# Kernel optimization log

Hardware: AMD Instinct MI355X
Metric: run time of the kernel (lower is better)

## Reference

```python
import jax, jax.numpy as jnp
import numpy as np

B, L, D, K = 16, 512, 512, 8
D2 = 2 * D
KS = 9
PAD = (KS - 1) // 2
EPS = 1e-5


def _conv_block(x, w, b, g, beta):
    # x: [B, L, D]; conv over time dim with 'same' padding, then LayerNorm over D, ReLU
    y = jax.lax.conv_general_dilated(
        x.transpose(0, 2, 1), w, window_strides=(1,), padding=[(PAD, PAD)],
        dimension_numbers=('NCH', 'OIH', 'NCH'))
    y = y.transpose(0, 2, 1) + b  # [B, L, D]
    mean = jnp.mean(y, axis=-1, keepdims=True)
    var = jnp.var(y, axis=-1, keepdims=True)
    y = (y - mean) * jax.lax.rsqrt(var + EPS) * g + beta
    return jax.nn.relu(y)


def _gru_scan(x, w_ih, w_hh, b_ih, b_hh):
    # x: [B, L, D]; torch GRUCell math, input = concat(x_t, h_{t-1}) per module
    def step(h, x_t):
        p = jnp.concatenate([x_t, h], axis=-1)          # [B, D + D2]
        gi = p @ w_ih.T + b_ih                          # [B, 3*D2]
        gh = h @ w_hh.T + b_hh
        ir, iz, inn = jnp.split(gi, 3, axis=-1)
        hr, hz, hn = jnp.split(gh, 3, axis=-1)
        r = jax.nn.sigmoid(ir + hr)
        z = jax.nn.sigmoid(iz + hz)
        n = jnp.tanh(inn + r * hn)
        h_new = (1.0 - z) * n + z * h
        return h_new, h_new

    h0 = jnp.zeros((x.shape[0], w_hh.shape[1]), x.dtype)
    _, hs = jax.lax.scan(step, h0, x.transpose(1, 0, 2))  # [L, B, D2]
    return hs.transpose(1, 0, 2)                           # [B, L, D2]


def setup_inputs() -> dict:
    key = jax.random.key(0)
    ks = jax.random.split(key, 12)
    n = lambda k, sh, s=0.02: jax.random.normal(k, sh, dtype=jnp.float32) * s
    return {
        'h_text': jax.random.normal(ks[0], (B, L, D), dtype=jnp.float32),
        'conv1_w': n(ks[1], (D, D, KS)), 'conv1_b': jnp.zeros((D,), jnp.float32),
        'ln1_g': jnp.ones((D,), jnp.float32), 'ln1_b': jnp.zeros((D,), jnp.float32),
        'conv2_w': n(ks[2], (D, D, KS)), 'conv2_b': jnp.zeros((D,), jnp.float32),
        'ln2_g': jnp.ones((D,), jnp.float32), 'ln2_b': jnp.zeros((D,), jnp.float32),
        'w_ih': n(ks[3], (3 * D2, D + D2)), 'w_hh': n(ks[4], (3 * D2, D2)),
        'b_ih': jnp.zeros((3 * D2,), jnp.float32), 'b_hh': jnp.zeros((3 * D2,), jnp.float32),
        'mdn_w_w': n(ks[5], (K, D2)), 'mdn_w_b': jnp.zeros((K,), jnp.float32),
        'mdn_sigma_w': n(ks[6], (K * D2, D2)), 'mdn_sigma_b': jnp.zeros((K * D2,), jnp.float32),
        'mdn_mu_w': n(ks[7], (K * D2, D2)), 'mdn_mu_b': jnp.zeros((K * D2,), jnp.float32),
    }


def reference(h_text, conv1_w, conv1_b, ln1_g, ln1_b, conv2_w, conv2_b, ln2_g, ln2_b,
              w_ih, w_hh, b_ih, b_hh, mdn_w_w, mdn_w_b, mdn_sigma_w, mdn_sigma_b,
              mdn_mu_w, mdn_mu_b):
    x = _conv_block(h_text, conv1_w, conv1_b, ln1_g, ln1_b)
    x = _conv_block(x, conv2_w, conv2_b, ln2_g, ln2_b)
    h = _gru_scan(x, w_ih, w_hh, b_ih, b_hh)                 # [B, L, 2D]
    w = jax.nn.softmax(h @ mdn_w_w.T + mdn_w_b, axis=-1)     # [B, L, K]
    sigma = jnp.exp(h @ mdn_sigma_w.T + mdn_sigma_b).reshape(B, L, K, D2)
    mu = (h @ mdn_mu_w.T + mdn_mu_b).reshape(B, L, K, D2)
    return (w, sigma, mu)
```

## Files before the change

kernel.cpp:

```cpp
#include <hip/hip_runtime.h>
#include <hip/hip_bf16.h>
#include <math.h>

#define BB 16
#define LL 512
#define DD 512
#define DD2 1024
#define KMIX 8
#define LPAD 520
#define GRU_KSTEPS 33

typedef __attribute__((ext_vector_type(8))) short short8;
typedef __attribute__((ext_vector_type(4))) float f32x4;
typedef unsigned short ushort;

__device__ __forceinline__ float bf2f(ushort u) {
  union { float f; unsigned i; } v; v.i = ((unsigned)u) << 16; return v.f;
}
__device__ __forceinline__ ushort f2bf(float f) {
  union { float f; unsigned i; } v; v.f = f;
  unsigned i = v.i;
  unsigned r = i + 0x7FFF + ((i >> 16) & 1);
  return (ushort)(r >> 16);
}

__global__ void k_zero_bf16(ushort* p, long n) {
  for (long i = blockIdx.x * 256 + threadIdx.x; i < n; i += (long)gridDim.x * 256) p[i] = 0;
}
__global__ void k_fill_xpad(const float* __restrict__ x, ushort* __restrict__ xp) {
  const long n = (long)BB * LPAD * DD;
  for (long i = blockIdx.x * 256 + threadIdx.x; i < n; i += (long)gridDim.x * 256) {
    int d = (int)(i & 511);
    long rest = i >> 9;
    int p = (int)(rest % LPAD);
    int b = (int)(rest / LPAD);
    float v = 0.f;
    if (p >= 4 && p < 516) v = x[((long)b * LL + (p - 4)) * DD + d];
    xp[i] = f2bf(v);
  }
}
__global__ void k_pack_convw(const float* __restrict__ w, ushort* __restrict__ wp) {
  const long n = (long)DD * DD * 9;
  for (long idx = blockIdx.x * 256 + threadIdx.x; idx < n; idx += (long)gridDim.x * 256) {
    int i = (int)(idx & 511);
    int o = (int)((idx >> 9) & 511);
    int k = (int)(idx >> 18);
    wp[idx] = f2bf(w[((long)o * DD + i) * 9 + k]);
  }
}
__global__ void k_pack_wihx(const float* __restrict__ w_ih, ushort* __restrict__ wp) {
  const long n = (long)3 * DD2 * DD;
  for (long idx = blockIdx.x * 256 + threadIdx.x; idx < n; idx += (long)gridDim.x * 256) {
    int i = (int)(idx & 511);
    int nr = (int)(idx >> 9);
    wp[idx] = f2bf(w_ih[(long)nr * 1536 + i]);
  }
}
__global__ void k_pack_bf16(const float* __restrict__ s, ushort* __restrict__ d, long n) {
  for (long i = blockIdx.x * 256 + threadIdx.x; i < n; i += (long)gridDim.x * 256) d[i] = f2bf(s[i]);
}
__global__ void k_pack_gru(const float* __restrict__ w_ih, const float* __restrict__ w_hh,
                           const float* __restrict__ b_hh, ushort* __restrict__ wp) {
  const long n = (long)64 * 6 * GRU_KSTEPS * 64 * 8;
  for (long idx = blockIdx.x * 256 + threadIdx.x; idx < n; idx += (long)gridDim.x * 256) {
    int j = (int)(idx & 7);
    int lane = (int)((idx >> 3) & 63);
    long r9 = idx >> 9;
    int ks = (int)(r9 % GRU_KSTEPS);
    long tmp = r9 / GRU_KSTEPS;
    int s = (int)(tmp % 6);
    int blk = (int)(tmp / 6);
    int k = ks * 32 + ((lane >> 4) << 3) + j;
    int u = blk * 16 + (lane & 15);
    float v = 0.f;
    if (s < 3) {
      if (k < 1024) v = w_ih[((long)(s * DD2 + u)) * 1536 + 512 + k];
    } else {
      int nr = (s - 3) * DD2 + u;
      if (k < 1024) v = w_hh[(long)nr * DD2 + k];
      else if (k == 1024) v = b_hh[nr];
    }
    wp[idx] = f2bf(v);
  }
}
__global__ void k_init_hbuf(ushort* hb, unsigned* flags) {
  int i = blockIdx.x * 256 + threadIdx.x;
  if (i < 16384) hb[i] = 0;
  if (i < 1024) flags[i] = 0u;
}

template <int MODE, int AMAP>
__global__ __launch_bounds__(256) void gemm128(
    const ushort* __restrict__ A, int lda, long segAoff,
    const ushort* __restrict__ Bt, int ldb, long segBoff,
    int nseg, int kseg, void* __restrict__ Cout, int ldc,
    const float* __restrict__ bias) {
  __shared__ ushort As[128 * 64];
  __shared__ ushort Bs[128 * 64];
  const int tid = threadIdx.x, lane = tid & 63, w = tid >> 6;
  const int wr = w >> 1, wc = w & 1;
  const int m0 = blockIdx.y * 128, n0 = blockIdx.x * 128;

  const ushort* Abase;
  if (AMAP == 1) {
    int b = m0 >> 9, l = m0 & 511;
    Abase = A + ((long)(b * LPAD + l)) * DD;
  } else {
    Abase = A + (long)m0 * lda;
  }
  const ushort* Bbase = Bt + (long)n0 * ldb;

  f32x4 acc[4][4];
#pragma unroll
  for (int i = 0; i < 4; i++)
#pragma unroll
    for (int j = 0; j < 4; j++) acc[i][j] = {0.f, 0.f, 0.f, 0.f};

  for (int seg = 0; seg < nseg; ++seg) {
    const ushort* Aseg = Abase + (long)seg * segAoff;
    const ushort* Bseg = Bbase + (long)seg * segBoff;
    for (int k0 = 0; k0 < kseg; k0 += 64) {
#pragma unroll
      for (int it = 0; it < 4; ++it) {
        int chunk = it * 256 + tid;
        int r = chunk >> 3, cc = chunk & 7;
        int sc = cc ^ (r & 7);
        *(short8*)&As[(size_t)chunk * 8] = *(const short8*)(Aseg + (long)r * lda + k0 + sc * 8);
        *(short8*)&Bs[(size_t)chunk * 8] = *(const short8*)(Bseg + (long)r * ldb + k0 + sc * 8);
      }
      __syncthreads();
#pragma unroll
      for (int kk = 0; kk < 2; ++kk) {
        short8 af[4], bfv[4];
#pragma unroll
        for (int m = 0; m < 4; m++) {
          int row = wr * 64 + m * 16 + (lane & 15);
          int ch = (kk * 4 + (lane >> 4)) ^ (row & 7);
          af[m] = *(const short8*)&As[(size_t)(row * 8 + ch) * 8];
        }
#pragma unroll
        for (int nn = 0; nn < 4; nn++) {
          int row = wc * 64 + nn * 16 + (lane & 15);
          int ch = (kk * 4 + (lane >> 4)) ^ (row & 7);
          bfv[nn] = *(const short8*)&Bs[(size_t)(row * 8 + ch) * 8];
        }
#pragma unroll
        for (int m = 0; m < 4; m++)
#pragma unroll
          for (int nn = 0; nn < 4; nn++)
            acc[m][nn] = __builtin_amdgcn_mfma_f32_16x16x32_bf16(af[m], bfv[nn], acc[m][nn], 0, 0, 0);
      }
      __syncthreads();
    }
  }
  float bvals[4];
#pragma unroll
  for (int nn = 0; nn < 4; nn++) {
    int c = n0 + wc * 64 + nn * 16 + (lane & 15);
    bvals[nn] = bias[c];
  }
#pragma unroll
  for (int m = 0; m < 4; m++) {
    int rbase = m0 + wr * 64 + m * 16 + ((lane >> 4) << 2);
#pragma unroll
    for (int nn = 0; nn < 4; nn++) {
      int c = n0 + wc * 64 + nn * 16 + (lane & 15);
#pragma unroll
      for (int j = 0; j < 4; j++) {
        float v = acc[m][nn][j] + bvals[nn];
        long off = (long)(rbase + j) * ldc + c;
        if (MODE == 0) ((float*)Cout)[off] = v;
        else {
          int r = rbase + j;
          int bb = r >> 9, tt = r & 511, ss = c >> 10, uu = c & 1023;
          long o2 = ((((long)(tt * 64 + (uu >> 4))) * 3 + ss) << 8) + (bb << 4) + (uu & 15);
          ((ushort*)Cout)[o2] = f2bf(v);
        }
      }
    }
  }
}

template <int DSTPAD>
__global__ __launch_bounds__(256) void ln_relu(
    const float* __restrict__ y, const float* __restrict__ g,
    const float* __restrict__ be, ushort* __restrict__ dst) {
  const int r = blockIdx.x, tid = threadIdx.x;
  float v0 = y[(long)r * DD + tid];
  float v1 = y[(long)r * DD + 256 + tid];
  float s = v0 + v1, sq = v0 * v0 + v1 * v1;
#pragma unroll
  for (int o = 32; o; o >>= 1) { s += __shfl_down(s, o); sq += __shfl_down(sq, o); }
  __shared__ float red[8];
  int w = tid >> 6, lane = tid & 63;
  if (lane == 0) { red[w] = s; red[4 + w] = sq; }
  __syncthreads();
  if (tid == 0) {
    float ts = 0.f, tq = 0.f;
#pragma unroll
    for (int i = 0; i < 4; i++) { ts += red[i]; tq += red[4 + i]; }
    red[0] = ts; red[1] = tq;
  }
  __syncthreads();
  float mean = red[0] * (1.f / 512.f);
  float var = red[1] * (1.f / 512.f) - mean * mean;
  float rs = rsqrtf(var + 1e-5f);
  long dbase;
  if (DSTPAD) { int b = r >> 9, l = r & 511; dbase = ((long)(b * LPAD + l + 4)) * DD; }
  else dbase = (long)r * DD;
  float o0 = fmaxf(0.f, (v0 - mean) * rs * g[tid] + be[tid]);
  float o1 = fmaxf(0.f, (v1 - mean) * rs * g[tid + 256] + be[tid + 256]);
  dst[dbase + tid] = f2bf(o0);
  dst[dbase + 256 + tid] = f2bf(o1);
}

__device__ __forceinline__ void wait_flags(unsigned need, int tid,
                                           const unsigned* __restrict__ flags) {
  if ((tid >> 6) == 0) {
    while (1) {
      unsigned f = __hip_atomic_load(&flags[(tid & 63) << 4], __ATOMIC_RELAXED,
                                     __HIP_MEMORY_SCOPE_AGENT);
      if (__all((int)(f >= need))) break;
      __builtin_amdgcn_s_sleep(127);
    }
  }
  __syncthreads();
}

__device__ void do_pair(int m0, int n0,
                        const ushort* __restrict__ A,
                        const ushort* __restrict__ Bsg, const ushort* __restrict__ Bmu,
                        const float* __restrict__ sg_b, const float* __restrict__ mu_b,
                        float* __restrict__ Cs, float* __restrict__ Cm,
                        char* smem, int tid) {
  ushort* As = (ushort*)smem;
  ushort* B1 = As + 128 * 64;
  ushort* B2 = B1 + 128 * 64;
  const int lane = tid & 63, w = tid >> 6;
  const int wr = w >> 2, wc = w & 3;
  const ushort* Abase = A + (long)m0 * DD2;
  const ushort* Bsb = Bsg + (long)n0 * DD2;
  const ushort* Bmb = Bmu + (long)n0 * DD2;
  f32x4 accS[4][2], accM[4][2];
#pragma unroll
  for (int m = 0; m < 4; m++)
#pragma unroll
    for (int n = 0; n < 2; n++) { accS[m][n] = {0.f,0.f,0.f,0.f}; accM[m][n] = {0.f,0.f,0.f,0.f}; }

  for (int k0 = 0; k0 < DD2; k0 += 64) {
#pragma unroll
    for (int it = 0; it < 2; ++it) {
      int chunk = it * 512 + tid;
      int r = chunk >> 3, cc = chunk & 7, sc = cc ^ (r & 7);
      *(short8*)&As[(size_t)chunk * 8] = *(const short8*)(Abase + (long)r * DD2 + k0 + sc * 8);
      *(short8*)&B1[(size_t)chunk * 8] = *(const short8*)(Bsb + (long)r * DD2 + k0 + sc * 8);
      *(short8*)&B2[(size_t)chunk * 8] = *(const short8*)(Bmb + (long)r * DD2 + k0 + sc * 8);
    }
    __syncthreads();
#pragma unroll
    for (int kk = 0; kk < 2; ++kk) {
      short8 af[4], b1[2], b2[2];
#pragma unroll
      for (int m = 0; m < 4; m++) {
        int row = wr * 64 + m * 16 + (lane & 15);
        int ch = (kk * 4 + (lane >> 4)) ^ (row & 7);
        af[m] = *(const short8*)&As[(size_t)(row * 8 + ch) * 8];
      }
#pragma unroll
      for (int n = 0; n < 2; n++) {
        int row = wc * 32 + n * 16 + (lane & 15);
        int ch = (kk * 4 + (lane >> 4)) ^ (row & 7);
        b1[n] = *(const short8*)&B1[(size_t)(row * 8 + ch) * 8];
        b2[n] = *(const short8*)&B2[(size_t)(row * 8 + ch) * 8];
      }
#pragma unroll
      for (int m = 0; m < 4; m++)
#pragma unroll
        for (int n = 0; n < 2; n++) {
          accS[m][n] = __builtin_amdgcn_mfma_f32_16x16x32_bf16(af[m], b1[n], accS[m][n], 0, 0, 0);
          accM[m][n] = __builtin_amdgcn_mfma_f32_16x16x32_bf16(af[m], b2[n], accM[m][n], 0, 0, 0);
        }
    }
    __syncthreads();
  }
  const int ldc = KMIX * DD2;
#pragma unroll
  for (int n = 0; n < 2; n++) {
    const int c = n0 + wc * 32 + n * 16 + (lane & 15);
    const float bs = sg_b[c], bm = mu_b[c];
#pragma unroll
    for (int m = 0; m < 4; m++) {
      const int rbase = m0 + wr * 64 + m * 16 + ((lane >> 4) << 2);
#pragma unroll
      for (int j = 0; j < 4; j++) {
        const long off = (long)(rbase + j) * ldc + c;
        Cs[off] = expf(accS[m][n][j] + bs);
        Cm[off] = accM[m][n][j] + bm;
      }
    }
  }
}

__global__ __launch_bounds__(512, 2) void fused_scan_mdn(
    const ushort* __restrict__ Wp, const ushort* __restrict__ gix2,
    const float* __restrict__ b_hh,
    ushort* __restrict__ hbuf, ushort* __restrict__ h_seq,
    unsigned* __restrict__ flags,
    const ushort* __restrict__ mdnsg, const ushort* __restrict__ mdnmu,
    const float* __restrict__ sg_b, const float* __restrict__ mu_b,
    float* __restrict__ outS, float* __restrict__ outM) {
  __shared__ char smem[49152];
  const int tid = threadIdx.x;

  if (blockIdx.x < 64) {
    float* red = (float*)smem;
    const int lane = tid & 63, w = tid >> 6, blk = blockIdx.x;
    const int j_c = w;
    const int u_local = lane & 15;
    const int b = ((lane >> 4) << 2) + (j_c & 3);
    const int u = (blk << 4) + u_local;
    const int lanep = ((blk & 1) * 2 + (u_local >> 3)) * 16 + b;
    const long hout_off = ((long)(blk >> 1) * 64 + lanep) * 8 + (u_local & 7);
    const ushort* wpw = Wp + (long)blk * 6 * GRU_KSTEPS * 512 + (long)lane * 8;
    const float bhr = b_hh[u], bhz = b_hh[DD2 + u], bhn = b_hh[2 * DD2 + u];
    float hold = 0.f;

    short8 wr0[4], wr1[4], wr2[4], wr3[4], wr4[4], wr5[4];
#pragma unroll
    for (int i = 0; i < 4; ++i) {
      const int ks = i * 8 + w;
      wr0[i] = *(const short8*)(wpw + (long)(0 * GRU_KSTEPS + ks) * 512);
      wr1[i] = *(const short8*)(wpw + (long)(1 * GRU_KSTEPS + ks) * 512);
      wr2[i] = *(const short8*)(wpw + (long)(2 * GRU_KSTEPS + ks) * 512);
      wr3[i] = *(const short8*)(wpw + (long)(3 * GRU_KSTEPS + ks) * 512);
      wr4[i] = *(const short8*)(wpw + (long)(4 * GRU_KSTEPS + ks) * 512);
      wr5[i] = *(const short8*)(wpw + (long)(5 * GRU_KSTEPS + ks) * 512);
    }

    const int gofs = (b << 4) + u_local;
    for (int t = 0; t < LL; ++t) {
      float gx_r = 0.f, gx_z = 0.f, gx_n = 0.f;
      if (w < 4) {
        const long gbase = ((long)(t * 64 + blk) * 3) << 8;
        gx_r = bf2f(__builtin_nontemporal_load(gix2 + gbase + gofs));
        gx_z = bf2f(__builtin_nontemporal_load(gix2 + gbase + 256 + gofs));
        gx_n = bf2f(__builtin_nontemporal_load(gix2 + gbase + 512 + gofs));
      }
      if (t > 0) {
        if (w == 0) {
          const unsigned tgt = (unsigned)t;
          while (1) {
            unsigned f = __hip_atomic_load(&flags[lane << 4], __ATOMIC_RELAXED,
                                           __HIP_MEMORY_SCOPE_AGENT);
            if (__all((int)(f >= tgt))) break;
            __builtin_amdgcn_s_sleep(1);
          }
        }
        __syncthreads();
      }

      const ushort* hb = hbuf + ((long)t << 14);
      f32x4 acc0 = {0.f,0.f,0.f,0.f}, acc1 = acc0, acc2 = acc0,
            acc3 = acc0, acc4 = acc0, acc5 = acc0;
#pragma unroll
      for (int i = 0; i < 4; ++i) {
        const int ks = i * 8 + w;
        unsigned long long* ap = (unsigned long long*)(hb + (((long)ks * 64 + lane) << 3));
        union { unsigned long long q[2]; short8 v; } cv;
        cv.q[0] = __hip_atomic_load(ap,     __ATOMIC_RELAXED, __HIP_MEMORY_SCOPE_AGENT);
        cv.q[1] = __hip_atomic_load(ap + 1, __ATOMIC_RELAXED, __HIP_MEMORY_SCOPE_AGENT);
        acc0 = __builtin_amdgcn_mfma_f32_16x16x32_bf16(cv.v, wr0[i], acc0, 0, 0, 0);
        acc1 = __builtin_amdgcn_mfma_f32_16x16x32_bf16(cv.v, wr1[i], acc1, 0, 0, 0);
        acc2 = __builtin_amdgcn_mfma_f32_16x16x32_bf16(cv.v, wr2[i], acc2, 0, 0, 0);
        acc3 = __builtin_amdgcn_mfma_f32_16x16x32_bf16(cv.v, wr3[i], acc3, 0, 0, 0);
        acc4 = __builtin_amdgcn_mfma_f32_16x16x32_bf16(cv.v, wr4[i], acc4, 0, 0, 0);
        acc5 = __builtin_amdgcn_mfma_f32_16x16x32_bf16(cv.v, wr5[i], acc5, 0, 0, 0);
      }
#pragma unroll
      for (int j = 0; j < 4; ++j) {
        red[((w * 6 + 0) << 8) + (j << 6) + lane] = acc0[j];
        red[((w * 6 + 1) << 8) + (j << 6) + lane] = acc1[j];
        red[((w * 6 + 2) << 8) + (j << 6) + lane] = acc2[j];
        red[((w * 6 + 3) << 8) + (j << 6) + lane] = acc3[j];
        red[((w * 6 + 4) << 8) + (j << 6) + lane] = acc4[j];
        red[((w * 6 + 5) << 8) + (j << 6) + lane] = acc5[j];
      }
      __syncthreads();
      ushort h16 = 0;
      if (w < 4) {
        float v0 = 0.f, v1 = 0.f, v2 = 0.f, v3 = 0.f, v4 = 0.f, v5 = 0.f;
#pragma unroll
        for (int wv = 0; wv < 8; ++wv) {
          const int base = ((wv * 6) << 8) + (j_c << 6) + lane;
          v0 += red[base];
          v1 += red[base + 256];
          v2 += red[base + 512];
          v3 += red[base + 768];
          v4 += red[base + 1024];
          v5 += red[base + 1280];
        }
        const float rg = 1.f / (1.f + __expf(-(gx_r + v0 + v3 + bhr)));
        const float zg = 1.f / (1.f + __expf(-(gx_z + v1 + v4 + bhz)));
        const float nx = gx_n + v2 + rg * (v5 + bhn);
        const float ng = 1.f - 2.f / (__expf(2.f * nx) + 1.f);
        const float hn = (1.f - zg) * ng + zg * hold;
        hold = hn;
        h16 = f2bf(hn);
      }
      if (t < LL - 1) {
        if (w < 4)
          __hip_atomic_store(hbuf + (((long)(t + 1)) << 14) + hout_off, h16,
                             __ATOMIC_RELAXED, __HIP_MEMORY_SCOPE_AGENT);
        __syncthreads();
        if (tid == 0)
          __hip_atomic_store(&flags[blk << 4], (unsigned)(t + 1), __ATOMIC_RELAXED,
                             __HIP_MEMORY_SCOPE_AGENT);
      }
      if (w < 4)
        __hip_atomic_store(h_seq + ((long)b * LL + t) * DD2 + u, h16,
                           __ATOMIC_RELAXED, __HIP_MEMORY_SCOPE_AGENT);
    }
    __syncthreads();
    if (tid == 0)
      __hip_atomic_store(&flags[blk << 4], 600u, __ATOMIC_RELAXED,
                         __HIP_MEMORY_SCOPE_AGENT);
  } else {
    const int wid = blockIdx.x - 64;
    for (int i = wid; i < 3072; i += 192) {
      const int nb = i & 63;
      const int rest = i >> 6;
      const int b = rest & 15;
      const int t0 = (rest >> 4) * 128;
      wait_flags((unsigned)(t0 + 129), tid, flags);
      do_pair(b * 512 + t0, nb * 128, h_seq, mdnsg, mdnmu, sg_b, mu_b,
              outS, outM, smem, tid);
    }
  }
  for (int i = blockIdx.x; i < 1024; i += 256) {
    const int nb = i & 63;
    const int b = (i >> 6) & 15;
    wait_flags(513u, tid, flags);
    do_pair(b * 512 + 384, nb * 128, h_seq, mdnsg, mdnmu, sg_b, mu_b,
            outS, outM, smem, tid);
  }
}

__global__ __launch_bounds__(256) void w_head(
    const ushort* __restrict__ h_seq, const float* __restrict__ ww,
    const float* __restrict__ wb, float* __restrict__ out) {
  const int tid = threadIdx.x, lane = tid & 63, w = tid >> 6;
  const long r = (long)blockIdx.x * 4 + w;
  float s[KMIX];
#pragma unroll
  for (int k = 0; k < KMIX; k++) s[k] = 0.f;
  for (int u = lane; u < DD2; u += 64) {
    float hv = bf2f(h_seq[r * DD2 + u]);
#pragma unroll
    for (int k = 0; k < KMIX; k++) s[k] += hv * ww[(long)k * DD2 + u];
  }
#pragma unroll
  for (int k = 0; k < KMIX; k++)
#pragma unroll
    for (int o = 32; o; o >>= 1) s[k] += __shfl_xor(s[k], o);
#pragma unroll
  for (int k = 0; k < KMIX; k++) s[k] += wb[k];
  float m = s[0];
#pragma unroll
  for (int k = 1; k < KMIX; k++) m = fmaxf(m, s[k]);
  float esum = 0.f;
#pragma unroll
  for (int k = 0; k < KMIX; k++) { s[k] = expf(s[k] - m); esum += s[k]; }
  float mine = 0.f;
#pragma unroll
  for (int k = 0; k < KMIX; k++) if (lane == k) mine = s[k];
  if (lane < KMIX) out[r * KMIX + lane] = mine / esum;
}

extern "C" void kernel_launch(void* const* d_in, const int* in_sizes, int n_in,
                              void* d_out, int out_size, void* d_ws, size_t ws_size,
                              hipStream_t stream) {
  const float* h_text     = (const float*)d_in[0];
  const float* conv1_w    = (const float*)d_in[1];
  const float* conv1_b    = (const float*)d_in[2];
  const float* ln1_g      = (const float*)d_in[3];
  const float* ln1_b      = (const float*)d_in[4];
  const float* conv2_w    = (const float*)d_in[5];
  const float* conv2_b    = (const float*)d_in[6];
  const float* ln2_g      = (const float*)d_in[7];
  const float* ln2_b      = (const float*)d_in[8];
  const float* w_ih       = (const float*)d_in[9];
  const float* w_hh       = (const float*)d_in[10];
  const float* b_ih       = (const float*)d_in[11];
  const float* b_hh       = (const float*)d_in[12];
  const float* mdn_w_w    = (const float*)d_in[13];
  const float* mdn_w_b    = (const float*)d_in[14];
  const float* mdn_sig_w  = (const float*)d_in[15];
  const float* mdn_sig_b  = (const float*)d_in[16];
  const float* mdn_mu_w   = (const float*)d_in[17];
  const float* mdn_mu_b   = (const float*)d_in[18];
  float* out = (float*)d_out;

  char* ws = (char*)d_ws;
  size_t off = 0;
  auto take = [&](size_t bytes) {
    void* p = ws + off;
    off += (bytes + 255) & ~(size_t)255;
    return p;
  };
  ushort* xpad1  = (ushort*)take((size_t)BB * LPAD * DD * 2);
  ushort* xpad2  = (ushort*)take((size_t)BB * LPAD * DD * 2);
  ushort* wpack1 = (ushort*)take((size_t)DD * DD * 9 * 2);
  ushort* wpack2 = (ushort*)take((size_t)DD * DD * 9 * 2);
  float*  ybuf   = (float*) take((size_t)BB * LL * DD * 4);
  ushort* x2     = (ushort*)take((size_t)BB * LL * DD * 2);
  ushort* wihx   = (ushort*)take((size_t)3 * DD2 * DD * 2);
  ushort* gix    = (ushort*)take((size_t)BB * LL * 3 * DD2 * 2);
  ushort* Wp     = (ushort*)take((size_t)64 * 6 * GRU_KSTEPS * 64 * 8 * 2);
  ushort* hseq   = (ushort*)take((size_t)BB * LL * DD2 * 2);
  ushort* mdnmu  = (ushort*)take((size_t)KMIX * DD2 * DD2 * 2);
  ushort* mdnsg  = (ushort*)take((size_t)KMIX * DD2 * DD2 * 2);
  ushort* hbuf   = (ushort*)take((size_t)512 * 16384 * 2);
  unsigned* flags = (unsigned*)take(64 * 16 * 4);

  const long sigma_off = (long)BB * LL * KMIX;
  const long mu_off    = sigma_off + (long)BB * LL * KMIX * DD2;

  k_fill_xpad<<<2048, 256, 0, stream>>>(h_text, xpad1);
  k_zero_bf16<<<2048, 256, 0, stream>>>(xpad2, (long)BB * LPAD * DD);
  k_pack_convw<<<2048, 256, 0, stream>>>(conv1_w, wpack1);
  k_pack_convw<<<2048, 256, 0, stream>>>(conv2_w, wpack2);
  k_pack_wihx<<<2048, 256, 0, stream>>>(w_ih, wihx);
  k_pack_gru<<<2048, 256, 0, stream>>>(w_ih, w_hh, b_hh, Wp);
  k_pack_bf16<<<2048, 256, 0, stream>>>(mdn_mu_w, mdnmu, (long)KMIX * DD2 * DD2);
  k_pack_bf16<<<2048, 256, 0, stream>>>(mdn_sig_w, mdnsg, (long)KMIX * DD2 * DD2);
  k_init_hbuf<<<64, 256, 0, stream>>>(hbuf, flags);

  gemm128<0, 1><<<dim3(4, 64), 256, 0, stream>>>(xpad1, DD, DD, wpack1, DD, (long)DD * DD, 9, DD,
                                                 ybuf, DD, conv1_b);
  ln_relu<1><<<BB * LL, 256, 0, stream>>>(ybuf, ln1_g, ln1_b, xpad2);

  gemm128<0, 1><<<dim3(4, 64), 256, 0, stream>>>(xpad2, DD, DD, wpack2, DD, (long)DD * DD, 9, DD,
                                                 ybuf, DD, conv2_b);
  ln_relu<0><<<BB * LL, 256, 0, stream>>>(ybuf, ln2_g, ln2_b, x2);

  gemm128<4, 0><<<dim3(24, 64), 256, 0, stream>>>(x2, DD, 0, wihx, DD, 0, 1, DD,
                                                  gix, 3 * DD2, b_ih);

  fused_scan_mdn<<<256, 512, 0, stream>>>(Wp, gix, b_hh, hbuf, hseq, flags,
                                          mdnsg, mdnmu, mdn_sig_b, mdn_mu_b,
                                          out + sigma_off, out + mu_off);

  w_head<<<BB * LL / 4, 256, 0, stream>>>(hseq, mdn_w_w, mdn_w_b, out);
}
```

Measured before the change: 1.696 ms.

## Split conv GEMM tiles, overlap final MDN chunk, fuse w-head into scan kernel

```diff
diff --git a/kernel.cpp b/kernel.cpp
--- a/kernel.cpp
+++ b/kernel.cpp
@@ -89,26 +89,89 @@
   if (i < 1024) flags[i] = 0u;
 }
 
-template <int MODE, int AMAP>
-__global__ __launch_bounds__(256) void gemm128(
-    const ushort* __restrict__ A, int lda, long segAoff,
-    const ushort* __restrict__ Bt, int ldb, long segBoff,
-    int nseg, int kseg, void* __restrict__ Cout, int ldc,
-    const float* __restrict__ bias) {
+__global__ __launch_bounds__(256) void conv_gemm(
+    const ushort* __restrict__ A, const ushort* __restrict__ Bt,
+    float* __restrict__ Cout, const float* __restrict__ bias) {
+  __shared__ ushort As[64 * 64];
+  __shared__ ushort Bs[128 * 64];
+  const int tid = threadIdx.x, lane = tid & 63, w = tid >> 6;
+  const int wr = w >> 1, wc = w & 1;
+  const int m0 = blockIdx.y * 64, n0 = blockIdx.x * 128;
+  const int b = m0 >> 9, l = m0 & 511;
+  const ushort* Abase = A + ((long)(b * LPAD + l)) * DD;
+  const ushort* Bbase = Bt + (long)n0 * DD;
+
+  f32x4 acc[2][4];
+#pragma unroll
+  for (int m = 0; m < 2; m++)
+#pragma unroll
+    for (int n = 0; n < 4; n++) acc[m][n] = {0.f, 0.f, 0.f, 0.f};
+
+  for (int seg = 0; seg < 9; ++seg) {
+    const ushort* Aseg = Abase + (long)seg * DD;
+    const ushort* Bseg = Bbase + (long)seg * DD * DD;
+    for (int k0 = 0; k0 < DD; k0 += 64) {
+#pragma unroll
+      for (int it = 0; it < 2; ++it) {
+        int chunk = it * 256 + tid;
+        int r = chunk >> 3, cc = chunk & 7, sc = cc ^ (r & 7);
+        *(short8*)&As[(size_t)chunk * 8] = *(const short8*)(Aseg + (long)r * DD + k0 + sc * 8);
+      }
+#pragma unroll
+      for (int it = 0; it < 4; ++it) {
+        int chunk = it * 256 + tid;
+        int r = chunk >> 3, cc = chunk & 7, sc = cc ^ (r & 7);
+        *(short8*)&Bs[(size_t)chunk * 8] = *(const short8*)(Bseg + (long)r * DD + k0 + sc * 8);
+      }
+      __syncthreads();
+#pragma unroll
+      for (int kk = 0; kk < 2; ++kk) {
+        short8 af[2], bfv[4];
+#pragma unroll
+        for (int m = 0; m < 2; m++) {
+          int row = wr * 32 + m * 16 + (lane & 15);
+          int ch = (kk * 4 + (lane >> 4)) ^ (row & 7);
+          af[m] = *(const short8*)&As[(size_t)(row * 8 + ch) * 8];
+        }
+#pragma unroll
+        for (int nn = 0; nn < 4; nn++) {
+          int row = wc * 64 + nn * 16 + (lane & 15);
+          int ch = (kk * 4 + (lane >> 4)) ^ (row & 7);
+          bfv[nn] = *(const short8*)&Bs[(size_t)(row * 8 + ch) * 8];
+        }
+#pragma unroll
+        for (int m = 0; m < 2; m++)
+#pragma unroll
+          for (int nn = 0; nn < 4; nn++)
+            acc[m][nn] = __builtin_amdgcn_mfma_f32_16x16x32_bf16(af[m], bfv[nn], acc[m][nn], 0, 0, 0);
+      }
+      __syncthreads();
+    }
+  }
+#pragma unroll
+  for (int nn = 0; nn < 4; nn++) {
+    const int c = n0 + wc * 64 + nn * 16 + (lane & 15);
+    const float bv = bias[c];
+#pragma unroll
+    for (int m = 0; m < 2; m++) {
+      const int rbase = m0 + wr * 32 + m * 16 + ((lane >> 4) << 2);
+#pragma unroll
+      for (int j = 0; j < 4; j++)
+        Cout[(long)(rbase + j) * DD + c] = acc[m][nn][j] + bv;
+    }
+  }
+}
+
+__global__ __launch_bounds__(256) void gix_gemm(
+    const ushort* __restrict__ A, const ushort* __restrict__ Bt,
+    ushort* __restrict__ Cout, const float* __restrict__ bias) {
   __shared__ ushort As[128 * 64];
   __shared__ ushort Bs[128 * 64];
   const int tid = threadIdx.x, lane = tid & 63, w = tid >> 6;
   const int wr = w >> 1, wc = w & 1;
   const int m0 = blockIdx.y * 128, n0 = blockIdx.x * 128;
-
-  const ushort* Abase;
-  if (AMAP == 1) {
-    int b = m0 >> 9, l = m0 & 511;
-    Abase = A + ((long)(b * LPAD + l)) * DD;
-  } else {
-    Abase = A + (long)m0 * lda;
-  }
-  const ushort* Bbase = Bt + (long)n0 * ldb;
+  const ushort* Abase = A + (long)m0 * DD;
+  const ushort* Bbase = Bt + (long)n0 * DD;
 
   f32x4 acc[4][4];
 #pragma unroll
@@ -116,48 +179,37 @@
 #pragma unroll
     for (int j = 0; j < 4; j++) acc[i][j] = {0.f, 0.f, 0.f, 0.f};
 
-  for (int seg = 0; seg < nseg; ++seg) {
-    const ushort* Aseg = Abase + (long)seg * segAoff;
-    const ushort* Bseg = Bbase + (long)seg * segBoff;
-    for (int k0 = 0; k0 < kseg; k0 += 64) {
-#pragma unroll
-      for (int it = 0; it < 4; ++it) {
-        int chunk = it * 256 + tid;
-        int r = chunk >> 3, cc = chunk & 7;
-        int sc = cc ^ (r & 7);
-        *(short8*)&As[(size_t)chunk * 8] = *(const short8*)(Aseg + (long)r * lda + k0 + sc * 8);
-        *(short8*)&Bs[(size_t)chunk * 8] = *(const short8*)(Bseg + (long)r * ldb + k0 + sc * 8);
-      }
-      __syncthreads();
-#pragma unroll
-      for (int kk = 0; kk < 2; ++kk) {
-        short8 af[4], bfv[4];
-#pragma unroll
-        for (int m = 0; m < 4; m++) {
-          int row = wr * 64 + m * 16 + (lane & 15);
-          int ch = (kk * 4 + (lane >> 4)) ^ (row & 7);
-          af[m] = *(const short8*)&As[(size_t)(row * 8 + ch) * 8];
-        }
-#pragma unroll
-        for (int nn = 0; nn < 4; nn++) {
-          int row = wc * 64 + nn * 16 + (lane & 15);
-          int ch = (kk * 4 + (lane >> 4)) ^ (row & 7);
-          bfv[nn] = *(const short8*)&Bs[(size_t)(row * 8 + ch) * 8];
-        }
-#pragma unroll
-        for (int m = 0; m < 4; m++)
-#pragma unroll
-          for (int nn = 0; nn < 4; nn++)
-            acc[m][nn] = __builtin_amdgcn_mfma_f32_16x16x32_bf16(af[m], bfv[nn], acc[m][nn], 0, 0, 0);
-      }
-      __syncthreads();
-    }
-  }
-  float bvals[4];
-#pragma unroll
-  for (int nn = 0; nn < 4; nn++) {
-    int c = n0 + wc * 64 + nn * 16 + (lane & 15);
-    bvals[nn] = bias[c];
+  for (int k0 = 0; k0 < DD; k0 += 64) {
+#pragma unroll
+    for (int it = 0; it < 4; ++it) {
+      int chunk = it * 256 + tid;
+      int r = chunk >> 3, cc = chunk & 7, sc = cc ^ (r & 7);
+      *(short8*)&As[(size_t)chunk * 8] = *(const short8*)(Abase + (long)r * DD + k0 + sc * 8);
+      *(short8*)&Bs[(size_t)chunk * 8] = *(const short8*)(Bbase + (long)r * DD + k0 + sc * 8);
+    }
+    __syncthreads();
+#pragma unroll
+    for (int kk = 0; kk < 2; ++kk) {
+      short8 af[4], bfv[4];
+#pragma unroll
+      for (int m = 0; m < 4; m++) {
+        int row = wr * 64 + m * 16 + (lane & 15);
+        int ch = (kk * 4 + (lane >> 4)) ^ (row & 7);
+        af[m] = *(const short8*)&As[(size_t)(row * 8 + ch) * 8];
+      }
+#pragma unroll
+      for (int nn = 0; nn < 4; nn++) {
+        int row = wc * 64 + nn * 16 + (lane & 15);
+        int ch = (kk * 4 + (lane >> 4)) ^ (row & 7);
+        bfv[nn] = *(const short8*)&Bs[(size_t)(row * 8 + ch) * 8];
+      }
+#pragma unroll
+      for (int m = 0; m < 4; m++)
+#pragma unroll
+        for (int nn = 0; nn < 4; nn++)
+          acc[m][nn] = __builtin_amdgcn_mfma_f32_16x16x32_bf16(af[m], bfv[nn], acc[m][nn], 0, 0, 0);
+    }
+    __syncthreads();
   }
 #pragma unroll
   for (int m = 0; m < 4; m++) {
@@ -165,17 +217,14 @@
 #pragma unroll
     for (int nn = 0; nn < 4; nn++) {
       int c = n0 + wc * 64 + nn * 16 + (lane & 15);
+      const float bv = bias[c];
 #pragma unroll
       for (int j = 0; j < 4; j++) {
-        float v = acc[m][nn][j] + bvals[nn];
-        long off = (long)(rbase + j) * ldc + c;
-        if (MODE == 0) ((float*)Cout)[off] = v;
-        else {
-          int r = rbase + j;
-          int bb = r >> 9, tt = r & 511, ss = c >> 10, uu = c & 1023;
-          long o2 = ((((long)(tt * 64 + (uu >> 4))) * 3 + ss) << 8) + (bb << 4) + (uu & 15);
-          ((ushort*)Cout)[o2] = f2bf(v);
-        }
+        float v = acc[m][nn][j] + bv;
+        int r = rbase + j;
+        int bb = r >> 9, tt = r & 511, ss = c >> 10, uu = c & 1023;
+        long o2 = ((((long)(tt * 64 + (uu >> 4))) * 3 + ss) << 8) + (bb << 4) + (uu & 15);
+        Cout[o2] = f2bf(v);
       }
     }
   }
@@ -227,39 +276,47 @@
   __syncthreads();
 }
 
+template <int MR>
 __device__ void do_pair(int m0, int n0,
                         const ushort* __restrict__ A,
                         const ushort* __restrict__ Bsg, const ushort* __restrict__ Bmu,
                         const float* __restrict__ sg_b, const float* __restrict__ mu_b,
                         float* __restrict__ Cs, float* __restrict__ Cm,
                         char* smem, int tid) {
+  constexpr int NF = (MR == 128) ? 2 : 1;
   ushort* As = (ushort*)smem;
-  ushort* B1 = As + 128 * 64;
+  ushort* B1 = As + MR * 64;
   ushort* B2 = B1 + 128 * 64;
   const int lane = tid & 63, w = tid >> 6;
-  const int wr = w >> 2, wc = w & 3;
+  const int wr = (MR == 128) ? (w >> 2) : 0;
+  const int wc = (MR == 128) ? (w & 3) : w;
   const ushort* Abase = A + (long)m0 * DD2;
   const ushort* Bsb = Bsg + (long)n0 * DD2;
   const ushort* Bmb = Bmu + (long)n0 * DD2;
-  f32x4 accS[4][2], accM[4][2];
+  f32x4 accS[4][NF], accM[4][NF];
 #pragma unroll
   for (int m = 0; m < 4; m++)
 #pragma unroll
-    for (int n = 0; n < 2; n++) { accS[m][n] = {0.f,0.f,0.f,0.f}; accM[m][n] = {0.f,0.f,0.f,0.f}; }
+    for (int n = 0; n < NF; n++) { accS[m][n] = {0.f,0.f,0.f,0.f}; accM[m][n] = {0.f,0.f,0.f,0.f}; }
 
   for (int k0 = 0; k0 < DD2; k0 += 64) {
+#pragma unroll
+    for (int it = 0; it < MR / 64; ++it) {
+      int chunk = it * 512 + tid;
+      int r = chunk >> 3, cc = chunk & 7, sc = cc ^ (r & 7);
+      *(short8*)&As[(size_t)chunk * 8] = *(const short8*)(Abase + (long)r * DD2 + k0 + sc * 8);
+    }
 #pragma unroll
     for (int it = 0; it < 2; ++it) {
       int chunk = it * 512 + tid;
       int r = chunk >> 3, cc = chunk & 7, sc = cc ^ (r & 7);
-      *(short8*)&As[(size_t)chunk * 8] = *(const short8*)(Abase + (long)r * DD2 + k0 + sc * 8);
       *(short8*)&B1[(size_t)chunk * 8] = *(const short8*)(Bsb + (long)r * DD2 + k0 + sc * 8);
       *(short8*)&B2[(size_t)chunk * 8] = *(const short8*)(Bmb + (long)r * DD2 + k0 + sc * 8);
     }
     __syncthreads();
 #pragma unroll
     for (int kk = 0; kk < 2; ++kk) {
-      short8 af[4], b1[2], b2[2];
+      short8 af[4], b1[NF], b2[NF];
 #pragma unroll
       for (int m = 0; m < 4; m++) {
         int row = wr * 64 + m * 16 + (lane & 15);
@@ -267,8 +324,8 @@
         af[m] = *(const short8*)&As[(size_t)(row * 8 + ch) * 8];
       }
 #pragma unroll
-      for (int n = 0; n < 2; n++) {
-        int row = wc * 32 + n * 16 + (lane & 15);
+      for (int n = 0; n < NF; n++) {
+        int row = wc * (16 * NF) + n * 16 + (lane & 15);
         int ch = (kk * 4 + (lane >> 4)) ^ (row & 7);
         b1[n] = *(const short8*)&B1[(size_t)(row * 8 + ch) * 8];
         b2[n] = *(const short8*)&B2[(size_t)(row * 8 + ch) * 8];
@@ -276,7 +333,7 @@
 #pragma unroll
       for (int m = 0; m < 4; m++)
 #pragma unroll
-        for (int n = 0; n < 2; n++) {
+        for (int n = 0; n < NF; n++) {
           accS[m][n] = __builtin_amdgcn_mfma_f32_16x16x32_bf16(af[m], b1[n], accS[m][n], 0, 0, 0);
           accM[m][n] = __builtin_amdgcn_mfma_f32_16x16x32_bf16(af[m], b2[n], accM[m][n], 0, 0, 0);
         }
@@ -285,8 +342,8 @@
   }
   const int ldc = KMIX * DD2;
 #pragma unroll
-  for (int n = 0; n < 2; n++) {
-    const int c = n0 + wc * 32 + n * 16 + (lane & 15);
+  for (int n = 0; n < NF; n++) {
+    const int c = n0 + wc * (16 * NF) + n * 16 + (lane & 15);
     const float bs = sg_b[c], bm = mu_b[c];
 #pragma unroll
     for (int m = 0; m < 4; m++) {
@@ -308,7 +365,9 @@
     unsigned* __restrict__ flags,
     const ushort* __restrict__ mdnsg, const ushort* __restrict__ mdnmu,
     const float* __restrict__ sg_b, const float* __restrict__ mu_b,
-    float* __restrict__ outS, float* __restrict__ outM) {
+    float* __restrict__ outS, float* __restrict__ outM,
+    const float* __restrict__ ww, const float* __restrict__ wb,
+    float* __restrict__ outW) {
   __shared__ char smem[49152];
   const int tid = threadIdx.x;
 
@@ -432,48 +491,56 @@
       const int b = rest & 15;
       const int t0 = (rest >> 4) * 128;
       wait_flags((unsigned)(t0 + 129), tid, flags);
-      do_pair(b * 512 + t0, nb * 128, h_seq, mdnsg, mdnmu, sg_b, mu_b,
-              outS, outM, smem, tid);
+      do_pair<128>(b * 512 + t0, nb * 128, h_seq, mdnsg, mdnmu, sg_b, mu_b,
+                   outS, outM, smem, tid);
+    }
+    for (int i = wid; i < 1024; i += 192) {
+      const int nb = i & 63;
+      const int b = (i >> 6) & 15;
+      wait_flags(449u, tid, flags);
+      do_pair<64>(b * 512 + 384, nb * 128, h_seq, mdnsg, mdnmu, sg_b, mu_b,
+                  outS, outM, smem, tid);
     }
   }
   for (int i = blockIdx.x; i < 1024; i += 256) {
     const int nb = i & 63;
     const int b = (i >> 6) & 15;
     wait_flags(513u, tid, flags);
-    do_pair(b * 512 + 384, nb * 128, h_seq, mdnsg, mdnmu, sg_b, mu_b,
-            outS, outM, smem, tid);
-  }
-}
-
-__global__ __launch_bounds__(256) void w_head(
-    const ushort* __restrict__ h_seq, const float* __restrict__ ww,
-    const float* __restrict__ wb, float* __restrict__ out) {
-  const int tid = threadIdx.x, lane = tid & 63, w = tid >> 6;
-  const long r = (long)blockIdx.x * 4 + w;
-  float s[KMIX];
-#pragma unroll
-  for (int k = 0; k < KMIX; k++) s[k] = 0.f;
-  for (int u = lane; u < DD2; u += 64) {
-    float hv = bf2f(h_seq[r * DD2 + u]);
-#pragma unroll
-    for (int k = 0; k < KMIX; k++) s[k] += hv * ww[(long)k * DD2 + u];
-  }
-#pragma unroll
-  for (int k = 0; k < KMIX; k++)
-#pragma unroll
-    for (int o = 32; o; o >>= 1) s[k] += __shfl_xor(s[k], o);
-#pragma unroll
-  for (int k = 0; k < KMIX; k++) s[k] += wb[k];
-  float m = s[0];
-#pragma unroll
-  for (int k = 1; k < KMIX; k++) m = fmaxf(m, s[k]);
-  float esum = 0.f;
-#pragma unroll
-  for (int k = 0; k < KMIX; k++) { s[k] = expf(s[k] - m); esum += s[k]; }
-  float mine = 0.f;
-#pragma unroll
-  for (int k = 0; k < KMIX; k++) if (lane == k) mine = s[k];
-  if (lane < KMIX) out[r * KMIX + lane] = mine / esum;
+    do_pair<64>(b * 512 + 448, nb * 128, h_seq, mdnsg, mdnmu, sg_b, mu_b,
+                outS, outM, smem, tid);
+  }
+  wait_flags(513u, tid, flags);
+  {
+    const int lane = tid & 63, w = tid >> 6;
+#pragma unroll
+    for (int i = 0; i < 4; ++i) {
+      const long r = (long)blockIdx.x * 32 + i * 8 + w;
+      float s[KMIX];
+#pragma unroll
+      for (int k = 0; k < KMIX; k++) s[k] = 0.f;
+      for (int u = lane; u < DD2; u += 64) {
+        float hv = bf2f(h_seq[r * DD2 + u]);
+#pragma unroll
+        for (int k = 0; k < KMIX; k++) s[k] += hv * ww[(long)k * DD2 + u];
+      }
+#pragma unroll
+      for (int k = 0; k < KMIX; k++)
+#pragma unroll
+        for (int o = 32; o; o >>= 1) s[k] += __shfl_xor(s[k], o);
+#pragma unroll
+      for (int k = 0; k < KMIX; k++) s[k] += wb[k];
+      float m = s[0];
+#pragma unroll
+      for (int k = 1; k < KMIX; k++) m = fmaxf(m, s[k]);
+      float esum = 0.f;
+#pragma unroll
+      for (int k = 0; k < KMIX; k++) { s[k] = expf(s[k] - m); esum += s[k]; }
+      float mine = 0.f;
+#pragma unroll
+      for (int k = 0; k < KMIX; k++) if (lane == k) mine = s[k];
+      if (lane < KMIX) outW[r * KMIX + lane] = mine / esum;
+    }
+  }
 }
 
 extern "C" void kernel_launch(void* const* d_in, const int* in_sizes, int n_in,
@@ -535,20 +602,16 @@
   k_pack_bf16<<<2048, 256, 0, stream>>>(mdn_sig_w, mdnsg, (long)KMIX * DD2 * DD2);
   k_init_hbuf<<<64, 256, 0, stream>>>(hbuf, flags);
 
-  gemm128<0, 1><<<dim3(4, 64), 256, 0, stream>>>(xpad1, DD, DD, wpack1, DD, (long)DD * DD, 9, DD,
-                                                 ybuf, DD, conv1_b);
+  conv_gemm<<<dim3(4, 128), 256, 0, stream>>>(xpad1, wpack1, ybuf, conv1_b);
   ln_relu<1><<<BB * LL, 256, 0, stream>>>(ybuf, ln1_g, ln1_b, xpad2);
 
-  gemm128<0, 1><<<dim3(4, 64), 256, 0, stream>>>(xpad2, DD, DD, wpack2, DD, (long)DD * DD, 9, DD,
-                                                 ybuf, DD, conv2_b);
+  conv_gemm<<<dim3(4, 128), 256, 0, stream>>>(xpad2, wpack2, ybuf, conv2_b);
   ln_relu<0><<<BB * LL, 256, 0, stream>>>(ybuf, ln2_g, ln2_b, x2);
 
-  gemm128<4, 0><<<dim3(24, 64), 256, 0, stream>>>(x2, DD, 0, wihx, DD, 0, 1, DD,
-                                                  gix, 3 * DD2, b_ih);
+  gix_gemm<<<dim3(24, 64), 256, 0, stream>>>(x2, wihx, gix, b_ih);
 
   fused_scan_mdn<<<256, 512, 0, stream>>>(Wp, gix, b_hh, hbuf, hseq, flags,
                                           mdnsg, mdnmu, mdn_sig_b, mdn_mu_b,
-                                          out + sigma_off, out + mu_off);
-
-  w_head<<<BB * LL / 4, 256, 0, stream>>>(hseq, mdn_w_w, mdn_w_b, out);
-}
+                                          out + sigma_off, out + mu_off,
+                                          mdn_w_w, mdn_w_b, out);
+}
```

Measured after the change: 1.682 ms. No clear change (-0.9%).
